# Optimization experiments

Hardware: AMD Instinct MI355X
Metric: run time of the kernel (lower is better)

Reference implementation:

```python
import jax, jax.numpy as jnp
import numpy as np

NUM_HEADS = 16
ROPE_BASE = 10000.0

def _rope(x):
    # x: (B, T, H, hd), rotate-half 1D RoPE over temporal axis
    B, T, H, hd = x.shape
    inv_freq = 1.0 / (ROPE_BASE ** (jnp.arange(0, hd, 2, dtype=jnp.float32) / hd))  # (hd/2,)
    freqs = jnp.arange(T, dtype=jnp.float32)[:, None] * inv_freq[None, :]            # (T, hd/2)
    emb = jnp.concatenate([freqs, freqs], axis=-1)                                    # (T, hd)
    cos = jnp.cos(emb)[None, :, None, :]
    sin = jnp.sin(emb)[None, :, None, :]
    x1, x2 = jnp.split(x, 2, axis=-1)
    rot = jnp.concatenate([-x2, x1], axis=-1)
    return x * cos + rot * sin

def setup_inputs() -> dict:
    key = jax.random.key(0)
    ks = jax.random.split(key, 7)
    B, T, S, D = 4, 16, 256, 2048
    std = 0.02
    return {
        'v_p': jax.random.normal(ks[0], (B, T, S, D), jnp.float32),
        'v_f': jax.random.normal(ks[1], (B, T, S, D), jnp.float32),
        'a_p': jax.random.normal(ks[2], (B, T, D), jnp.float32),
        'a_f': jax.random.normal(ks[3], (B, T, D), jnp.float32),
        'W_qkv': jax.random.normal(ks[4], (D, 3 * D), jnp.float32) * std,
        'W_proj': jax.random.normal(ks[5], (D, D), jnp.float32) * std,
        'b_proj': jnp.zeros((D,), jnp.float32),
    }

def reference(v_p, v_f, a_p, a_f, W_qkv, W_proj, b_proj):
    B, T_p, S, D = v_p.shape
    T_f = v_f.shape[1]
    H = NUM_HEADS
    hd = D // H
    scale = hd ** -0.5
    # pool spatial dim and concatenate streams: [v_p, v_f, a_p, a_f]
    tokens = jnp.concatenate([v_p.mean(axis=2), v_f.mean(axis=2), a_p, a_f], axis=1)  # (B, T, D)
    T = tokens.shape[1]
    qkv = tokens @ W_qkv  # qkv_bias=False
    q, k, v = jnp.split(qkv, 3, axis=-1)
    q = q.reshape(B, T, H, hd)
    k = k.reshape(B, T, H, hd)
    v = v.reshape(B, T, H, hd)
    q = _rope(q)
    k = _rope(k)
    scores = jnp.einsum('bqhd,bkhd->bhqk', q, k) * scale
    causal_mask = jnp.triu(jnp.ones((T, T), dtype=bool), k=1)
    scores = jnp.where(causal_mask[None, None], -jnp.inf, scores)
    attn = jax.nn.softmax(scores, axis=-1)
    out = jnp.einsum('bhqk,bkhd->bqhd', attn, v).reshape(B, T, D)
    out = out @ W_proj + b_proj
    v_p_out = jnp.broadcast_to(out[:, :T_p, None, :], (B, T_p, S, D))
    v_f_out = jnp.broadcast_to(out[:, T_p:T_p + T_f, None, :], (B, T_f, S, D))
    a_p_out = out[:, T_p + T_f:T_p + T_f + T_p]
    a_f_out = out[:, T_p + T_f + T_p:]
    return (v_p_out, v_f_out, a_p_out, a_f_out)
```

## Files before the change

kernel.cpp:

```cpp
#include <hip/hip_runtime.h>
#include <hip/hip_bf16.h>
#include <stdint.h>


using bf16x8v = __attribute__((ext_vector_type(8))) __bf16;
using f32x4v  = __attribute__((ext_vector_type(4))) float;

union Pack8 { __bf16 h[8]; uint4 u; };

__device__ __forceinline__ int swz(int r, int c) {
    return (r << 6) + (((c ^ (r & 7))) << 3);
}

__global__ __launch_bounds__(256) void prep_w_kernel(
    const float* __restrict__ src, __bf16* __restrict__ dst, int N)
{
    __shared__ float Ls[64][68];
    int tiles_n = N >> 6;
    int tn = blockIdx.x % tiles_n;
    int tk = blockIdx.x / tiles_n;
    int t = threadIdx.x;
    int rb = t >> 4;
    int c4 = (t & 15) << 2;
    #pragma unroll
    for (int s = 0; s < 4; ++s) {
        int r = rb + (s << 4);
        float4 v = *reinterpret_cast<const float4*>(
            src + (size_t)(tk * 64 + r) * N + tn * 64 + c4);
        *reinterpret_cast<float4*>(&Ls[r][c4]) = v;
    }
    __syncthreads();
    int c  = t >> 2;
    int r0 = (t & 3) << 4;
    Pack8 p0, p1;
    #pragma unroll
    for (int i = 0; i < 8; ++i) p0.h[i] = (__bf16)Ls[r0 + i][c];
    #pragma unroll
    for (int i = 0; i < 8; ++i) p1.h[i] = (__bf16)Ls[r0 + 8 + i][c];
    __bf16* drow = dst + (size_t)(tn * 64 + c) * 2048 + tk * 64 + r0;
    *reinterpret_cast<uint4*>(drow)     = p0.u;
    *reinterpret_cast<uint4*>(drow + 8) = p1.u;
}

__global__ __launch_bounds__(256) void mean_stage1_kernel(
    const float* __restrict__ v_p, const float* __restrict__ v_f,
    float* __restrict__ partials)
{
    int bid = blockIdx.x;
    int which  = bid >> 9;
    int rem    = bid & 511;
    int row    = rem >> 3;
    int dchunk = (rem >> 2) & 1;
    int schunk = rem & 3;
    int d = (dchunk << 10) + (threadIdx.x << 2);
    const float* src = (which ? v_f : v_p) + ((size_t)row << 19)
                     + ((size_t)(schunk << 6) << 11) + d;
    float4 a = {0.f, 0.f, 0.f, 0.f};
    #pragma unroll 8
    for (int s = 0; s < 64; ++s) {
        float4 x = *reinterpret_cast<const float4*>(src + ((size_t)s << 11));
        a.x += x.x; a.y += x.y; a.z += x.z; a.w += x.w;
    }
    int pr = which * 64 + row;
    *reinterpret_cast<float4*>(&partials[(size_t)((pr << 2) + schunk) * 2048 + d]) = a;
}

__global__ __launch_bounds__(256) void mean_stage2_kernel(
    const float* __restrict__ partials, __bf16* __restrict__ tokens_bf)
{
    int idx = (blockIdx.x * 256 + threadIdx.x) * 8;
    int r = idx >> 11;
    int d = idx & 2047;
    float s[8];
    #pragma unroll
    for (int i = 0; i < 8; ++i) s[i] = 0.f;
    #pragma unroll
    for (int sc = 0; sc < 4; ++sc) {
        const float* p = partials + (size_t)((r << 2) + sc) * 2048 + d;
        float4 x0 = *reinterpret_cast<const float4*>(p);
        float4 x1 = *reinterpret_cast<const float4*>(p + 4);
        s[0] += x0.x; s[1] += x0.y; s[2] += x0.z; s[3] += x0.w;
        s[4] += x1.x; s[5] += x1.y; s[6] += x1.z; s[7] += x1.w;
    }
    const float inv = 1.f / 256.f;
    int which = r >> 6, rr = r & 63;
    int b = rr >> 4, tt = rr & 15;
    int tokrow = b * 64 + which * 16 + tt;
    Pack8 p;
    #pragma unroll
    for (int i = 0; i < 8; ++i) p.h[i] = (__bf16)(s[i] * inv);
    *reinterpret_cast<uint4*>(&tokens_bf[(size_t)tokrow * 2048 + d]) = p.u;
}

__global__ __launch_bounds__(256) void pack_audio_kernel(
    const float* __restrict__ a_p, const float* __restrict__ a_f,
    __bf16* __restrict__ tokens_bf)
{
    int g = blockIdx.x * 256 + threadIdx.x;
    int which = g >> 14;
    int j = g & 16383;
    int b = j >> 12;
    int rr = j & 4095;
    int tt = rr >> 8;
    int gq = rr & 255;
    const float* src = (which ? a_f : a_p) + (size_t)(b * 16 + tt) * 2048 + gq * 8;
    float4 x0 = *reinterpret_cast<const float4*>(src);
    float4 x1 = *reinterpret_cast<const float4*>(src + 4);
    Pack8 p;
    p.h[0] = (__bf16)x0.x; p.h[1] = (__bf16)x0.y; p.h[2] = (__bf16)x0.z; p.h[3] = (__bf16)x0.w;
    p.h[4] = (__bf16)x1.x; p.h[5] = (__bf16)x1.y; p.h[6] = (__bf16)x1.z; p.h[7] = (__bf16)x1.w;
    int tokrow = b * 64 + 32 + which * 16 + tt;
    *reinterpret_cast<uint4*>(&tokens_bf[(size_t)tokrow * 2048 + gq * 8]) = p.u;
}

__global__ __launch_bounds__(256) void gemm_bf16_kernel(
    const __bf16* __restrict__ A, const __bf16* __restrict__ Bt,
    const float* __restrict__ bias, float* __restrict__ C, int N)
{
    __shared__ __bf16 As[4096];
    __shared__ __bf16 Bs[4096];
    const int t = threadIdx.x;
    const int m0 = blockIdx.y << 6;
    const int n0 = blockIdx.x << 6;
    const int lane = t & 63;
    const int wm = (t >> 6) << 4;
    const int lrow = lane & 15;
    const int lk = lane >> 4;
    const int srow = t >> 3;
    const int sc = t & 7;
    const __bf16* gA = A  + (size_t)(m0 + srow) * 2048 + (sc << 3);
    const __bf16* gB = Bt + (size_t)(n0 + srow) * 2048 + (sc << 3);
    const int wA0 = swz(srow, sc), wA1 = swz(srow + 32, sc);

    f32x4v acc[4] = {{0.f,0.f,0.f,0.f},{0.f,0.f,0.f,0.f},
                     {0.f,0.f,0.f,0.f},{0.f,0.f,0.f,0.f}};
    uint4 pa0, pa1, pb0, pb1;
    pa0 = *reinterpret_cast<const uint4*>(gA);
    pa1 = *reinterpret_cast<const uint4*>(gA + 32 * 2048);
    pb0 = *reinterpret_cast<const uint4*>(gB);
    pb1 = *reinterpret_cast<const uint4*>(gB + 32 * 2048);

    for (int kt = 0; kt < 32; ++kt) {
        __syncthreads();
        *reinterpret_cast<uint4*>(&As[wA0]) = pa0;
        *reinterpret_cast<uint4*>(&As[wA1]) = pa1;
        *reinterpret_cast<uint4*>(&Bs[wA0]) = pb0;
        *reinterpret_cast<uint4*>(&Bs[wA1]) = pb1;
        __syncthreads();
        if (kt < 31) {
            const __bf16* nA = gA + (kt + 1) * 64;
            const __bf16* nB = gB + (kt + 1) * 64;
            pa0 = *reinterpret_cast<const uint4*>(nA);
            pa1 = *reinterpret_cast<const uint4*>(nA + 32 * 2048);
            pb0 = *reinterpret_cast<const uint4*>(nB);
            pb1 = *reinterpret_cast<const uint4*>(nB + 32 * 2048);
        }
        #pragma unroll
        for (int s = 0; s < 2; ++s) {
            int cA = (s << 2) + lk;
            bf16x8v af = *reinterpret_cast<const bf16x8v*>(&As[swz(wm + lrow, cA)]);
            #pragma unroll
            for (int j = 0; j < 4; ++j) {
                bf16x8v bf = *reinterpret_cast<const bf16x8v*>(&Bs[swz((j << 4) + lrow, cA)]);
                acc[j] = __builtin_amdgcn_mfma_f32_16x16x32_bf16(af, bf, acc[j], 0, 0, 0);
            }
        }
    }
    #pragma unroll
    for (int j = 0; j < 4; ++j) {
        int col = n0 + (j << 4) + lrow;
        float bv = bias ? bias[col] : 0.f;
        #pragma unroll
        for (int e = 0; e < 4; ++e) {
            int row = m0 + wm + (lk << 2) + e;
            C[(size_t)row * N + col] = acc[j][e] + bv;
        }
    }
}

__global__ __launch_bounds__(256) void rope_kernel(float* __restrict__ qkv)
{
    int row = blockIdx.x;
    int t = row & 63;
    float* q = qkv + (size_t)row * 6144;
    for (int i = threadIdx.x; i < 1024; i += 256) {
        int h = i >> 6;
        int d = i & 63;
        float invf = powf(10000.f, -(float)d * (1.f / 64.f));
        float ang = (float)t * invf;
        float c = cosf(ang), s = sinf(ang);
        int i0 = h * 128 + d;
        float q1 = q[i0], q2 = q[i0 + 64];
        q[i0]      = q1 * c - q2 * s;
        q[i0 + 64] = q2 * c + q1 * s;
        float* k = q + 2048;
        float k1 = k[i0], k2 = k[i0 + 64];
        k[i0]      = k1 * c - k2 * s;
        k[i0 + 64] = k2 * c + k1 * s;
    }
}

__global__ __launch_bounds__(256) void attn_kernel(
    const float* __restrict__ qkv, __bf16* __restrict__ attn_out)
{
    __shared__ float q_s[64 * 128];
    __shared__ float k_s[64 * 128];
    int b = blockIdx.x >> 4;
    int h = blockIdx.x & 15;
    int tid = threadIdx.x;
    const float* base = qkv + (size_t)(b * 64) * 6144 + h * 128;
    #pragma unroll
    for (int r = 0; r < 8; ++r) {
        int idx = tid + (r << 8);
        int t = idx >> 5;
        int d = (idx & 31) << 2;
        const float* src = base + (size_t)t * 6144 + d;
        *reinterpret_cast<float4*>(&q_s[t * 128 + d]) = *reinterpret_cast<const float4*>(src);
        *reinterpret_cast<float4*>(&k_s[t * 128 + d]) = *reinterpret_cast<const float4*>(src + 2048);
    }
    __syncthreads();
    int qi = tid >> 2;
    int g  = tid & 3;
    float pv[16];
    #pragma unroll
    for (int j = 0; j < 16; ++j) pv[j] = 0.f;
    for (int d = 0; d < 128; d += 4) {
        float4 a = *reinterpret_cast<const float4*>(&q_s[qi * 128 + d]);
        #pragma unroll
        for (int j = 0; j < 16; ++j) {
            int ki = (j << 2) + g;
            float4 bb = *reinterpret_cast<const float4*>(&k_s[ki * 128 + d]);
            pv[j] += a.x * bb.x + a.y * bb.y + a.z * bb.z + a.w * bb.w;
        }
    }
    const float scale = 0.0883883476483184405f;
    float m = -1e30f;
    #pragma unroll
    for (int j = 0; j < 16; ++j) {
        int ki = (j << 2) + g;
        pv[j] = (ki <= qi) ? pv[j] * scale : -1e30f;
        m = fmaxf(m, pv[j]);
    }
    m = fmaxf(m, __shfl_xor(m, 1));
    m = fmaxf(m, __shfl_xor(m, 2));
    float l = 0.f;
    #pragma unroll
    for (int j = 0; j < 16; ++j) {
        float e = (pv[j] > -1e29f) ? expf(pv[j] - m) : 0.f;
        pv[j] = e;
        l += e;
    }
    l += __shfl_xor(l, 1);
    l += __shfl_xor(l, 2);
    float inv_l = 1.f / l;
    __syncthreads();
    float* p_s = q_s;
    #pragma unroll
    for (int j = 0; j < 16; ++j) p_s[qi * 65 + (j << 2) + g] = pv[j] * inv_l;
    float* v_s = k_s;
    #pragma unroll
    for (int r = 0; r < 8; ++r) {
        int idx = tid + (r << 8);
        int t = idx >> 5;
        int d = (idx & 31) << 2;
        *reinterpret_cast<float4*>(&v_s[t * 128 + d]) =
            *reinterpret_cast<const float4*>(base + (size_t)t * 6144 + 4096 + d);
    }
    __syncthreads();
    int d0 = g << 5;
    float4 acc[8];
    #pragma unroll
    for (int u = 0; u < 8; ++u) acc[u] = {0.f, 0.f, 0.f, 0.f};
    for (int ki = 0; ki < 64; ++ki) {
        float p = p_s[qi * 65 + ki];
        #pragma unroll
        for (int u = 0; u < 8; ++u) {
            float4 vv = *reinterpret_cast<const float4*>(&v_s[ki * 128 + d0 + (u << 2)]);
            acc[u].x += p * vv.x;
            acc[u].y += p * vv.y;
            acc[u].z += p * vv.z;
            acc[u].w += p * vv.w;
        }
    }
    __bf16* orow = attn_out + (size_t)(b * 64 + qi) * 2048 + h * 128 + d0;
    #pragma unroll
    for (int v = 0; v < 4; ++v) {
        Pack8 p;
        float4 a0 = acc[2 * v], a1 = acc[2 * v + 1];
        p.h[0] = (__bf16)a0.x; p.h[1] = (__bf16)a0.y; p.h[2] = (__bf16)a0.z; p.h[3] = (__bf16)a0.w;
        p.h[4] = (__bf16)a1.x; p.h[5] = (__bf16)a1.y; p.h[6] = (__bf16)a1.z; p.h[7] = (__bf16)a1.w;
        *reinterpret_cast<uint4*>(orow + v * 8) = p.u;
    }
}

__global__ __launch_bounds__(256) void bcast_video_kernel(
    const float* __restrict__ outp, float* __restrict__ d_out)
{
    int bid = blockIdx.x;
    int which = bid >> 10;
    int rem = bid & 1023;
    int row = rem >> 4;
    int schunk = rem & 15;
    int b = row >> 4;
    int t = row & 15;
    const float* src = outp + (size_t)(b * 64 + (which << 4) + t) * 2048 + threadIdx.x * 8;
    float4 o0 = *reinterpret_cast<const float4*>(src);
    float4 o1 = *reinterpret_cast<const float4*>(src + 4);
    size_t base = (size_t)which * 33554432 +
                  ((size_t)row * 256 + (size_t)schunk * 16) * 2048 + threadIdx.x * 8;
    float* dst = d_out + base;
    #pragma unroll
    for (int s = 0; s < 16; ++s) {
        *reinterpret_cast<float4*>(dst + (size_t)s * 2048)     = o0;
        *reinterpret_cast<float4*>(dst + (size_t)s * 2048 + 4) = o1;
    }
}

__global__ __launch_bounds__(256) void audio_out_kernel(
    const float* __restrict__ outp, float* __restrict__ d_out)
{
    int i = blockIdx.x * 256 + threadIdx.x;
    int which = i >> 15;
    int j = i & 32767;
    int b = j >> 13;
    int r = j & 8191;
    int t = r >> 9;
    int gq = r & 511;
    const float* src = outp + (size_t)(b * 64 + 32 + (which << 4) + t) * 2048 + gq * 4;
    float4 v = *reinterpret_cast<const float4*>(src);
    float* dst = d_out + 67108864 + (size_t)which * 131072 +
                 (size_t)(b * 16 + t) * 2048 + gq * 4;
    *reinterpret_cast<float4*>(dst) = v;
}

extern "C" void kernel_launch(void* const* d_in, const int* in_sizes, int n_in,
                              void* d_out, int out_size, void* d_ws, size_t ws_size,
                              hipStream_t stream)
{
    const float* v_p    = (const float*)d_in[0];
    const float* v_f    = (const float*)d_in[1];
    const float* a_p    = (const float*)d_in[2];
    const float* a_f    = (const float*)d_in[3];
    const float* W_qkv  = (const float*)d_in[4];
    const float* W_proj = (const float*)d_in[5];
    const float* b_proj = (const float*)d_in[6];
    float* out_f = (float*)d_out;

    char* ws = (char*)d_ws;
    __bf16* tokens_bf = (__bf16*)(ws);
    __bf16* Wt_qkv    = (__bf16*)(ws + 1048576);
    __bf16* Wt_proj   = (__bf16*)(ws + 26214400);
    float*  qkv       = (float*)(ws + 34603008);
    __bf16* attn_bf   = (__bf16*)(ws + 40894464);
    float*  outp      = (float*)(ws + 41943040);
    float*  partials  = (float*)(ws + 44040192);

    prep_w_kernel<<<3072, 256, 0, stream>>>(W_qkv, Wt_qkv, 6144);
    prep_w_kernel<<<1024, 256, 0, stream>>>(W_proj, Wt_proj, 2048);
    mean_stage1_kernel<<<1024, 256, 0, stream>>>(v_p, v_f, partials);
    mean_stage2_kernel<<<128, 256, 0, stream>>>(partials, tokens_bf);
    pack_audio_kernel<<<128, 256, 0, stream>>>(a_p, a_f, tokens_bf);
    gemm_bf16_kernel<<<dim3(96, 4), 256, 0, stream>>>(tokens_bf, Wt_qkv, nullptr, qkv, 6144);
    rope_kernel<<<256, 256, 0, stream>>>(qkv);
    attn_kernel<<<64, 256, 0, stream>>>(qkv, attn_bf);
    gemm_bf16_kernel<<<dim3(32, 4), 256, 0, stream>>>(attn_bf, Wt_proj, b_proj, outp, 2048);
    bcast_video_kernel<<<2048, 256, 0, stream>>>(outp, out_f);
    audio_out_kernel<<<256, 256, 0, stream>>>(outp, out_f);
}
```

Measured before the change: 245.8 us.

## Merge small kernels, fuse RoPE into QKV GEMM, split attention by query tile

Several launches are merged: the two weight prep kernels become one, mean stage2 and audio pack become one, and the video broadcast and audio output kernels become one. RoPE now runs in the QKV GEMM epilogue, which uses a 128-wide N tile so each block holds both halves of a head. Attention is split into two query tiles per (b,h), with causal key capping and V loaded up front. Mean stage1 uses twice as many blocks with shorter S chunks. The aim is less launch overhead, no separate RoPE pass over qkv, and more parallelism, at the cost of fewer GEMM blocks and more partials traffic.

```diff
diff --git a/kernel.cpp b/kernel.cpp
--- a/kernel.cpp
+++ b/kernel.cpp
@@ -9,16 +9,21 @@
 union Pack8 { __bf16 h[8]; uint4 u; };
 
 __device__ __forceinline__ int swz(int r, int c) {
-    return (r << 6) + (((c ^ (r & 7))) << 3);
+    return (r << 6) + ((c ^ (r & 7)) << 3);
 }
 
 __global__ __launch_bounds__(256) void prep_w_kernel(
-    const float* __restrict__ src, __bf16* __restrict__ dst, int N)
-{
+    const float* __restrict__ W_qkv, const float* __restrict__ W_proj,
+    __bf16* __restrict__ Wt_qkv, __bf16* __restrict__ Wt_proj)
+{
+    int bid = blockIdx.x;
+    const float* src; __bf16* dst; int N, tile;
+    if (bid < 3072) { src = W_qkv;  dst = Wt_qkv;  N = 6144; tile = bid; }
+    else            { src = W_proj; dst = Wt_proj; N = 2048; tile = bid - 3072; }
     __shared__ float Ls[64][68];
     int tiles_n = N >> 6;
-    int tn = blockIdx.x % tiles_n;
-    int tk = blockIdx.x / tiles_n;
+    int tn = tile % tiles_n;
+    int tk = tile / tiles_n;
     int t = threadIdx.x;
     int rb = t >> 4;
     int c4 = (t & 15) << 2;
@@ -47,81 +52,83 @@
     float* __restrict__ partials)
 {
     int bid = blockIdx.x;
-    int which  = bid >> 9;
-    int rem    = bid & 511;
-    int row    = rem >> 3;
-    int dchunk = (rem >> 2) & 1;
-    int schunk = rem & 3;
+    int which  = bid >> 10;
+    int rem    = bid & 1023;
+    int row    = rem >> 4;
+    int dchunk = (rem >> 3) & 1;
+    int schunk = rem & 7;
     int d = (dchunk << 10) + (threadIdx.x << 2);
     const float* src = (which ? v_f : v_p) + ((size_t)row << 19)
-                     + ((size_t)(schunk << 6) << 11) + d;
+                     + ((size_t)(schunk << 5) << 11) + d;
     float4 a = {0.f, 0.f, 0.f, 0.f};
     #pragma unroll 8
-    for (int s = 0; s < 64; ++s) {
+    for (int s = 0; s < 32; ++s) {
         float4 x = *reinterpret_cast<const float4*>(src + ((size_t)s << 11));
         a.x += x.x; a.y += x.y; a.z += x.z; a.w += x.w;
     }
     int pr = which * 64 + row;
-    *reinterpret_cast<float4*>(&partials[(size_t)((pr << 2) + schunk) * 2048 + d]) = a;
-}
-
-__global__ __launch_bounds__(256) void mean_stage2_kernel(
-    const float* __restrict__ partials, __bf16* __restrict__ tokens_bf)
-{
-    int idx = (blockIdx.x * 256 + threadIdx.x) * 8;
-    int r = idx >> 11;
-    int d = idx & 2047;
-    float s[8];
-    #pragma unroll
-    for (int i = 0; i < 8; ++i) s[i] = 0.f;
-    #pragma unroll
-    for (int sc = 0; sc < 4; ++sc) {
-        const float* p = partials + (size_t)((r << 2) + sc) * 2048 + d;
-        float4 x0 = *reinterpret_cast<const float4*>(p);
-        float4 x1 = *reinterpret_cast<const float4*>(p + 4);
-        s[0] += x0.x; s[1] += x0.y; s[2] += x0.z; s[3] += x0.w;
-        s[4] += x1.x; s[5] += x1.y; s[6] += x1.z; s[7] += x1.w;
-    }
-    const float inv = 1.f / 256.f;
-    int which = r >> 6, rr = r & 63;
-    int b = rr >> 4, tt = rr & 15;
-    int tokrow = b * 64 + which * 16 + tt;
-    Pack8 p;
-    #pragma unroll
-    for (int i = 0; i < 8; ++i) p.h[i] = (__bf16)(s[i] * inv);
-    *reinterpret_cast<uint4*>(&tokens_bf[(size_t)tokrow * 2048 + d]) = p.u;
-}
-
-__global__ __launch_bounds__(256) void pack_audio_kernel(
-    const float* __restrict__ a_p, const float* __restrict__ a_f,
-    __bf16* __restrict__ tokens_bf)
-{
-    int g = blockIdx.x * 256 + threadIdx.x;
-    int which = g >> 14;
-    int j = g & 16383;
-    int b = j >> 12;
-    int rr = j & 4095;
-    int tt = rr >> 8;
-    int gq = rr & 255;
-    const float* src = (which ? a_f : a_p) + (size_t)(b * 16 + tt) * 2048 + gq * 8;
-    float4 x0 = *reinterpret_cast<const float4*>(src);
-    float4 x1 = *reinterpret_cast<const float4*>(src + 4);
-    Pack8 p;
-    p.h[0] = (__bf16)x0.x; p.h[1] = (__bf16)x0.y; p.h[2] = (__bf16)x0.z; p.h[3] = (__bf16)x0.w;
-    p.h[4] = (__bf16)x1.x; p.h[5] = (__bf16)x1.y; p.h[6] = (__bf16)x1.z; p.h[7] = (__bf16)x1.w;
-    int tokrow = b * 64 + 32 + which * 16 + tt;
-    *reinterpret_cast<uint4*>(&tokens_bf[(size_t)tokrow * 2048 + gq * 8]) = p.u;
-}
-
+    *reinterpret_cast<float4*>(&partials[(size_t)((pr << 3) + schunk) * 2048 + d]) = a;
+}
+
+__global__ __launch_bounds__(256) void tokens_finish_kernel(
+    const float* __restrict__ partials, const float* __restrict__ a_p,
+    const float* __restrict__ a_f, __bf16* __restrict__ tokens_bf)
+{
+    int bid = blockIdx.x;
+    if (bid < 128) {
+        int idx = (bid * 256 + threadIdx.x) * 8;
+        int r = idx >> 11;
+        int d = idx & 2047;
+        float s[8];
+        #pragma unroll
+        for (int i = 0; i < 8; ++i) s[i] = 0.f;
+        #pragma unroll
+        for (int sc = 0; sc < 8; ++sc) {
+            const float* p = partials + (size_t)((r << 3) + sc) * 2048 + d;
+            float4 x0 = *reinterpret_cast<const float4*>(p);
+            float4 x1 = *reinterpret_cast<const float4*>(p + 4);
+            s[0] += x0.x; s[1] += x0.y; s[2] += x0.z; s[3] += x0.w;
+            s[4] += x1.x; s[5] += x1.y; s[6] += x1.z; s[7] += x1.w;
+        }
+        const float inv = 1.f / 256.f;
+        int which = r >> 6, rr = r & 63;
+        int b = rr >> 4, tt = rr & 15;
+        int tokrow = b * 64 + which * 16 + tt;
+        Pack8 p;
+        #pragma unroll
+        for (int i = 0; i < 8; ++i) p.h[i] = (__bf16)(s[i] * inv);
+        *reinterpret_cast<uint4*>(&tokens_bf[(size_t)tokrow * 2048 + d]) = p.u;
+    } else {
+        int g = (bid - 128) * 256 + threadIdx.x;
+        int which = g >> 14;
+        int j = g & 16383;
+        int b = j >> 12;
+        int rr = j & 4095;
+        int tt = rr >> 8;
+        int gq = rr & 255;
+        const float* src = (which ? a_f : a_p) + (size_t)(b * 16 + tt) * 2048 + gq * 8;
+        float4 x0 = *reinterpret_cast<const float4*>(src);
+        float4 x1 = *reinterpret_cast<const float4*>(src + 4);
+        Pack8 p;
+        p.h[0] = (__bf16)x0.x; p.h[1] = (__bf16)x0.y; p.h[2] = (__bf16)x0.z; p.h[3] = (__bf16)x0.w;
+        p.h[4] = (__bf16)x1.x; p.h[5] = (__bf16)x1.y; p.h[6] = (__bf16)x1.z; p.h[7] = (__bf16)x1.w;
+        int tokrow = b * 64 + 32 + which * 16 + tt;
+        *reinterpret_cast<uint4*>(&tokens_bf[(size_t)tokrow * 2048 + gq * 8]) = p.u;
+    }
+}
+
+template<int BN, bool ROPE>
 __global__ __launch_bounds__(256) void gemm_bf16_kernel(
     const __bf16* __restrict__ A, const __bf16* __restrict__ Bt,
     const float* __restrict__ bias, float* __restrict__ C, int N)
 {
+    constexpr int NJ = BN / 16;
+    constexpr int NR = BN / 32;
     __shared__ __bf16 As[4096];
-    __shared__ __bf16 Bs[4096];
+    __shared__ __bf16 Bs[BN * 64];
     const int t = threadIdx.x;
     const int m0 = blockIdx.y << 6;
-    const int n0 = blockIdx.x << 6;
+    const int n0 = blockIdx.x * BN;
     const int lane = t & 63;
     const int wm = (t >> 6) << 4;
     const int lrow = lane & 15;
@@ -130,44 +137,65 @@
     const int sc = t & 7;
     const __bf16* gA = A  + (size_t)(m0 + srow) * 2048 + (sc << 3);
     const __bf16* gB = Bt + (size_t)(n0 + srow) * 2048 + (sc << 3);
-    const int wA0 = swz(srow, sc), wA1 = swz(srow + 32, sc);
-
-    f32x4v acc[4] = {{0.f,0.f,0.f,0.f},{0.f,0.f,0.f,0.f},
-                     {0.f,0.f,0.f,0.f},{0.f,0.f,0.f,0.f}};
-    uint4 pa0, pa1, pb0, pb1;
-    pa0 = *reinterpret_cast<const uint4*>(gA);
-    pa1 = *reinterpret_cast<const uint4*>(gA + 32 * 2048);
-    pb0 = *reinterpret_cast<const uint4*>(gB);
-    pb1 = *reinterpret_cast<const uint4*>(gB + 32 * 2048);
+
+    f32x4v acc[NJ];
+    #pragma unroll
+    for (int j = 0; j < NJ; ++j) acc[j] = {0.f, 0.f, 0.f, 0.f};
+
+    uint4 pa[2], pb[NR];
+    pa[0] = *reinterpret_cast<const uint4*>(gA);
+    pa[1] = *reinterpret_cast<const uint4*>(gA + 32 * 2048);
+    #pragma unroll
+    for (int r = 0; r < NR; ++r)
+        pb[r] = *reinterpret_cast<const uint4*>(gB + (size_t)(r * 32) * 2048);
 
     for (int kt = 0; kt < 32; ++kt) {
         __syncthreads();
-        *reinterpret_cast<uint4*>(&As[wA0]) = pa0;
-        *reinterpret_cast<uint4*>(&As[wA1]) = pa1;
-        *reinterpret_cast<uint4*>(&Bs[wA0]) = pb0;
-        *reinterpret_cast<uint4*>(&Bs[wA1]) = pb1;
+        *reinterpret_cast<uint4*>(&As[swz(srow, sc)])      = pa[0];
+        *reinterpret_cast<uint4*>(&As[swz(srow + 32, sc)]) = pa[1];
+        #pragma unroll
+        for (int r = 0; r < NR; ++r)
+            *reinterpret_cast<uint4*>(&Bs[swz(srow + r * 32, sc)]) = pb[r];
         __syncthreads();
         if (kt < 31) {
             const __bf16* nA = gA + (kt + 1) * 64;
             const __bf16* nB = gB + (kt + 1) * 64;
-            pa0 = *reinterpret_cast<const uint4*>(nA);
-            pa1 = *reinterpret_cast<const uint4*>(nA + 32 * 2048);
-            pb0 = *reinterpret_cast<const uint4*>(nB);
-            pb1 = *reinterpret_cast<const uint4*>(nB + 32 * 2048);
+            pa[0] = *reinterpret_cast<const uint4*>(nA);
+            pa[1] = *reinterpret_cast<const uint4*>(nA + 32 * 2048);
+            #pragma unroll
+            for (int r = 0; r < NR; ++r)
+                pb[r] = *reinterpret_cast<const uint4*>(nB + (size_t)(r * 32) * 2048);
         }
         #pragma unroll
         for (int s = 0; s < 2; ++s) {
             int cA = (s << 2) + lk;
             bf16x8v af = *reinterpret_cast<const bf16x8v*>(&As[swz(wm + lrow, cA)]);
             #pragma unroll
-            for (int j = 0; j < 4; ++j) {
+            for (int j = 0; j < NJ; ++j) {
                 bf16x8v bf = *reinterpret_cast<const bf16x8v*>(&Bs[swz((j << 4) + lrow, cA)]);
                 acc[j] = __builtin_amdgcn_mfma_f32_16x16x32_bf16(af, bf, acc[j], 0, 0, 0);
             }
         }
     }
-    #pragma unroll
-    for (int j = 0; j < 4; ++j) {
+    if (ROPE && n0 < 4096) {
+        const float l2 = 0.20762050593046012f;
+        #pragma unroll
+        for (int j = 0; j < 4; ++j) {
+            int dd = (j << 4) + lrow;
+            float invf = exp2f(-(float)dd * l2);
+            #pragma unroll
+            for (int e = 0; e < 4; ++e) {
+                int row = m0 + wm + (lk << 2) + e;
+                float ang = (float)(row & 63) * invf;
+                float cc = cosf(ang), ss = sinf(ang);
+                float x1 = acc[j][e], x2 = acc[j + 4][e];
+                acc[j][e]     = x1 * cc - x2 * ss;
+                acc[j + 4][e] = x2 * cc + x1 * ss;
+            }
+        }
+    }
+    #pragma unroll
+    for (int j = 0; j < NJ; ++j) {
         int col = n0 + (j << 4) + lrow;
         float bv = bias ? bias[col] : 0.f;
         #pragma unroll
@@ -178,103 +206,83 @@
     }
 }
 
-__global__ __launch_bounds__(256) void rope_kernel(float* __restrict__ qkv)
-{
-    int row = blockIdx.x;
-    int t = row & 63;
-    float* q = qkv + (size_t)row * 6144;
-    for (int i = threadIdx.x; i < 1024; i += 256) {
-        int h = i >> 6;
-        int d = i & 63;
-        float invf = powf(10000.f, -(float)d * (1.f / 64.f));
-        float ang = (float)t * invf;
-        float c = cosf(ang), s = sinf(ang);
-        int i0 = h * 128 + d;
-        float q1 = q[i0], q2 = q[i0 + 64];
-        q[i0]      = q1 * c - q2 * s;
-        q[i0 + 64] = q2 * c + q1 * s;
-        float* k = q + 2048;
-        float k1 = k[i0], k2 = k[i0 + 64];
-        k[i0]      = k1 * c - k2 * s;
-        k[i0 + 64] = k2 * c + k1 * s;
-    }
-}
-
 __global__ __launch_bounds__(256) void attn_kernel(
     const float* __restrict__ qkv, __bf16* __restrict__ attn_out)
 {
-    __shared__ float q_s[64 * 128];
+    __shared__ float q_s[32 * 128];
     __shared__ float k_s[64 * 128];
-    int b = blockIdx.x >> 4;
-    int h = blockIdx.x & 15;
+    __shared__ float v_s[64 * 128];
+    int bid = blockIdx.x;
+    int qt = bid & 1;
+    int h  = (bid >> 1) & 15;
+    int b  = bid >> 5;
     int tid = threadIdx.x;
     const float* base = qkv + (size_t)(b * 64) * 6144 + h * 128;
-    #pragma unroll
-    for (int r = 0; r < 8; ++r) {
+    int qr0 = qt << 5;
+    int kcap = qr0 + 32;
+    #pragma unroll
+    for (int r = 0; r < 4; ++r) {
         int idx = tid + (r << 8);
-        int t = idx >> 5;
+        int tq = idx >> 5;
         int d = (idx & 31) << 2;
-        const float* src = base + (size_t)t * 6144 + d;
-        *reinterpret_cast<float4*>(&q_s[t * 128 + d]) = *reinterpret_cast<const float4*>(src);
-        *reinterpret_cast<float4*>(&k_s[t * 128 + d]) = *reinterpret_cast<const float4*>(src + 2048);
+        *reinterpret_cast<float4*>(&q_s[tq * 128 + d]) =
+            *reinterpret_cast<const float4*>(base + (size_t)(qr0 + tq) * 6144 + d);
+    }
+    for (int idx = tid; idx < (kcap << 5); idx += 256) {
+        int tk = idx >> 5;
+        int d = (idx & 31) << 2;
+        const float* srck = base + (size_t)tk * 6144 + 2048 + d;
+        *reinterpret_cast<float4*>(&k_s[tk * 128 + d]) = *reinterpret_cast<const float4*>(srck);
+        *reinterpret_cast<float4*>(&v_s[tk * 128 + d]) = *reinterpret_cast<const float4*>(srck + 2048);
     }
     __syncthreads();
-    int qi = tid >> 2;
-    int g  = tid & 3;
-    float pv[16];
-    #pragma unroll
-    for (int j = 0; j < 16; ++j) pv[j] = 0.f;
+    int qi = tid >> 3;
+    int g  = tid & 7;
+    int qg = qr0 + qi;
+    int nj = kcap >> 3;
+    float pv[8];
+    #pragma unroll
+    for (int j = 0; j < 8; ++j) pv[j] = 0.f;
     for (int d = 0; d < 128; d += 4) {
         float4 a = *reinterpret_cast<const float4*>(&q_s[qi * 128 + d]);
-        #pragma unroll
-        for (int j = 0; j < 16; ++j) {
-            int ki = (j << 2) + g;
+        for (int j = 0; j < nj; ++j) {
+            int ki = (j << 3) + g;
             float4 bb = *reinterpret_cast<const float4*>(&k_s[ki * 128 + d]);
             pv[j] += a.x * bb.x + a.y * bb.y + a.z * bb.z + a.w * bb.w;
         }
     }
     const float scale = 0.0883883476483184405f;
     float m = -1e30f;
-    #pragma unroll
-    for (int j = 0; j < 16; ++j) {
-        int ki = (j << 2) + g;
-        pv[j] = (ki <= qi) ? pv[j] * scale : -1e30f;
+    for (int j = 0; j < nj; ++j) {
+        int ki = (j << 3) + g;
+        pv[j] = (ki <= qg) ? pv[j] * scale : -1e30f;
         m = fmaxf(m, pv[j]);
     }
     m = fmaxf(m, __shfl_xor(m, 1));
     m = fmaxf(m, __shfl_xor(m, 2));
+    m = fmaxf(m, __shfl_xor(m, 4));
     float l = 0.f;
-    #pragma unroll
-    for (int j = 0; j < 16; ++j) {
+    for (int j = 0; j < nj; ++j) {
         float e = (pv[j] > -1e29f) ? expf(pv[j] - m) : 0.f;
         pv[j] = e;
         l += e;
     }
     l += __shfl_xor(l, 1);
     l += __shfl_xor(l, 2);
+    l += __shfl_xor(l, 4);
     float inv_l = 1.f / l;
     __syncthreads();
     float* p_s = q_s;
-    #pragma unroll
-    for (int j = 0; j < 16; ++j) p_s[qi * 65 + (j << 2) + g] = pv[j] * inv_l;
-    float* v_s = k_s;
-    #pragma unroll
-    for (int r = 0; r < 8; ++r) {
-        int idx = tid + (r << 8);
-        int t = idx >> 5;
-        int d = (idx & 31) << 2;
-        *reinterpret_cast<float4*>(&v_s[t * 128 + d]) =
-            *reinterpret_cast<const float4*>(base + (size_t)t * 6144 + 4096 + d);
-    }
+    for (int j = 0; j < nj; ++j) p_s[qi * 65 + (j << 3) + g] = pv[j] * inv_l;
     __syncthreads();
-    int d0 = g << 5;
-    float4 acc[8];
-    #pragma unroll
-    for (int u = 0; u < 8; ++u) acc[u] = {0.f, 0.f, 0.f, 0.f};
-    for (int ki = 0; ki < 64; ++ki) {
+    int d0 = g << 4;
+    float4 acc[4];
+    #pragma unroll
+    for (int u = 0; u < 4; ++u) acc[u] = {0.f, 0.f, 0.f, 0.f};
+    for (int ki = 0; ki < kcap; ++ki) {
         float p = p_s[qi * 65 + ki];
         #pragma unroll
-        for (int u = 0; u < 8; ++u) {
+        for (int u = 0; u < 4; ++u) {
             float4 vv = *reinterpret_cast<const float4*>(&v_s[ki * 128 + d0 + (u << 2)]);
             acc[u].x += p * vv.x;
             acc[u].y += p * vv.y;
@@ -282,9 +290,9 @@
             acc[u].w += p * vv.w;
         }
     }
-    __bf16* orow = attn_out + (size_t)(b * 64 + qi) * 2048 + h * 128 + d0;
-    #pragma unroll
-    for (int v = 0; v < 4; ++v) {
+    __bf16* orow = attn_out + (size_t)(b * 64 + qg) * 2048 + h * 128 + d0;
+    #pragma unroll
+    for (int v = 0; v < 2; ++v) {
         Pack8 p;
         float4 a0 = acc[2 * v], a1 = acc[2 * v + 1];
         p.h[0] = (__bf16)a0.x; p.h[1] = (__bf16)a0.y; p.h[2] = (__bf16)a0.z; p.h[3] = (__bf16)a0.w;
@@ -293,44 +301,44 @@
     }
 }
 
-__global__ __launch_bounds__(256) void bcast_video_kernel(
+__global__ __launch_bounds__(256) void outputs_kernel(
     const float* __restrict__ outp, float* __restrict__ d_out)
 {
     int bid = blockIdx.x;
-    int which = bid >> 10;
-    int rem = bid & 1023;
-    int row = rem >> 4;
-    int schunk = rem & 15;
-    int b = row >> 4;
-    int t = row & 15;
-    const float* src = outp + (size_t)(b * 64 + (which << 4) + t) * 2048 + threadIdx.x * 8;
-    float4 o0 = *reinterpret_cast<const float4*>(src);
-    float4 o1 = *reinterpret_cast<const float4*>(src + 4);
-    size_t base = (size_t)which * 33554432 +
-                  ((size_t)row * 256 + (size_t)schunk * 16) * 2048 + threadIdx.x * 8;
-    float* dst = d_out + base;
-    #pragma unroll
-    for (int s = 0; s < 16; ++s) {
-        *reinterpret_cast<float4*>(dst + (size_t)s * 2048)     = o0;
-        *reinterpret_cast<float4*>(dst + (size_t)s * 2048 + 4) = o1;
-    }
-}
-
-__global__ __launch_bounds__(256) void audio_out_kernel(
-    const float* __restrict__ outp, float* __restrict__ d_out)
-{
-    int i = blockIdx.x * 256 + threadIdx.x;
-    int which = i >> 15;
-    int j = i & 32767;
-    int b = j >> 13;
-    int r = j & 8191;
-    int t = r >> 9;
-    int gq = r & 511;
-    const float* src = outp + (size_t)(b * 64 + 32 + (which << 4) + t) * 2048 + gq * 4;
-    float4 v = *reinterpret_cast<const float4*>(src);
-    float* dst = d_out + 67108864 + (size_t)which * 131072 +
-                 (size_t)(b * 16 + t) * 2048 + gq * 4;
-    *reinterpret_cast<float4*>(dst) = v;
+    if (bid < 2048) {
+        int which = bid >> 10;
+        int rem = bid & 1023;
+        int row = rem >> 4;
+        int schunk = rem & 15;
+        int b = row >> 4;
+        int t = row & 15;
+        const float* src = outp + (size_t)(b * 64 + (which << 4) + t) * 2048 + threadIdx.x * 8;
+        float4 o0 = *reinterpret_cast<const float4*>(src);
+        float4 o1 = *reinterpret_cast<const float4*>(src + 4);
+        size_t base = (size_t)which * 33554432 +
+                      ((size_t)row * 256 + (size_t)schunk * 16) * 2048 + threadIdx.x * 8;
+        float* dst = d_out + base;
+        #pragma unroll
+        for (int s = 0; s < 16; ++s) {
+            *reinterpret_cast<float4*>(dst + (size_t)s * 2048)     = o0;
+            *reinterpret_cast<float4*>(dst + (size_t)s * 2048 + 4) = o1;
+        }
+    } else {
+        int g = (bid - 2048) * 256 + threadIdx.x;
+        int which = g >> 14;
+        int j = g & 16383;
+        int b = j >> 12;
+        int rr = j & 4095;
+        int tt = rr >> 8;
+        int gq = rr & 255;
+        const float* src = outp + (size_t)(b * 64 + 32 + (which << 4) + tt) * 2048 + gq * 8;
+        float4 x0 = *reinterpret_cast<const float4*>(src);
+        float4 x1 = *reinterpret_cast<const float4*>(src + 4);
+        float* dst = d_out + 67108864 + (size_t)which * 131072 +
+                     (size_t)(b * 16 + tt) * 2048 + gq * 8;
+        *reinterpret_cast<float4*>(dst)     = x0;
+        *reinterpret_cast<float4*>(dst + 4) = x1;
+    }
 }
 
 extern "C" void kernel_launch(void* const* d_in, const int* in_sizes, int n_in,
@@ -355,15 +363,11 @@
     float*  outp      = (float*)(ws + 41943040);
     float*  partials  = (float*)(ws + 44040192);
 
-    prep_w_kernel<<<3072, 256, 0, stream>>>(W_qkv, Wt_qkv, 6144);
-    prep_w_kernel<<<1024, 256, 0, stream>>>(W_proj, Wt_proj, 2048);
-    mean_stage1_kernel<<<1024, 256, 0, stream>>>(v_p, v_f, partials);
-    mean_stage2_kernel<<<128, 256, 0, stream>>>(partials, tokens_bf);
-    pack_audio_kernel<<<128, 256, 0, stream>>>(a_p, a_f, tokens_bf);
-    gemm_bf16_kernel<<<dim3(96, 4), 256, 0, stream>>>(tokens_bf, Wt_qkv, nullptr, qkv, 6144);
-    rope_kernel<<<256, 256, 0, stream>>>(qkv);
-    attn_kernel<<<64, 256, 0, stream>>>(qkv, attn_bf);
-    gemm_bf16_kernel<<<dim3(32, 4), 256, 0, stream>>>(attn_bf, Wt_proj, b_proj, outp, 2048);
-    bcast_video_kernel<<<2048, 256, 0, stream>>>(outp, out_f);
-    audio_out_kernel<<<256, 256, 0, stream>>>(outp, out_f);
-}
+    prep_w_kernel<<<4096, 256, 0, stream>>>(W_qkv, W_proj, Wt_qkv, Wt_proj);
+    mean_stage1_kernel<<<2048, 256, 0, stream>>>(v_p, v_f, partials);
+    tokens_finish_kernel<<<256, 256, 0, stream>>>(partials, a_p, a_f, tokens_bf);
+    gemm_bf16_kernel<128, true><<<dim3(48, 4), 256, 0, stream>>>(tokens_bf, Wt_qkv, nullptr, qkv, 6144);
+    attn_kernel<<<128, 256, 0, stream>>>(qkv, attn_bf);
+    gemm_bf16_kernel<64, false><<<dim3(32, 4), 256, 0, stream>>>(attn_bf, Wt_proj, b_proj, outp, 2048);
+    outputs_kernel<<<2176, 256, 0, stream>>>(outp, out_f);
+}
```

New measurement: 389.7 us. +58.6%, slower.
